# Optimization experiments

Hardware: AMD Instinct MI355X
Metric: run time of the kernel (lower is better)

The kernel has to match this reference:

```python
import jax, jax.numpy as jnp
import numpy as np

EMBED = 768
E2 = EMBED // 2  # 384
B = 128
T = 256   # 16x16 search tokens
T1 = 64   # 8x8 template tokens
EPS = 1e-5


def setup_inputs() -> dict:
    key = jax.random.key(0)
    ks = jax.random.split(key, 8)
    s = 0.02
    return {
        "z_r": jax.random.normal(ks[0], (B, T1, EMBED), jnp.float32),
        "z_i": jax.random.normal(ks[1], (B, T1, EMBED), jnp.float32),
        "x_r": jax.random.normal(ks[2], (B, T, EMBED), jnp.float32),
        "x_i": jax.random.normal(ks[3], (B, T, EMBED), jnp.float32),
        "fz_w": jax.random.normal(ks[4], (E2, 2 * EMBED), jnp.float32) * s,
        "fz_b": jnp.zeros((E2,), jnp.float32),
        "ln_g": jnp.ones((E2,), jnp.float32),
        "ln_b": jnp.zeros((E2,), jnp.float32),
        "wr": jax.random.normal(ks[5], (E2, EMBED, 3, 3), jnp.float32) * s,
        "br": jnp.zeros((E2,), jnp.float32),
        "bnr_g": jnp.ones((E2,), jnp.float32),
        "bnr_b": jnp.zeros((E2,), jnp.float32),
        "bnr_m": jnp.zeros((E2,), jnp.float32),
        "bnr_v": jnp.ones((E2,), jnp.float32),
        "wi": jax.random.normal(ks[6], (E2, EMBED, 3, 3), jnp.float32) * s,
        "bi": jnp.zeros((E2,), jnp.float32),
        "bni_g": jnp.ones((E2,), jnp.float32),
        "bni_b": jnp.zeros((E2,), jnp.float32),
        "bni_m": jnp.zeros((E2,), jnp.float32),
        "bni_v": jnp.ones((E2,), jnp.float32),
        "c": jnp.ones((1,), jnp.float32) * E2,
    }


def _gelu(x):
    return jax.nn.gelu(x, approximate=False)


def _layernorm(x, g, b):
    mu = jnp.mean(x, axis=-1, keepdims=True)
    var = jnp.mean(jnp.square(x - mu), axis=-1, keepdims=True)
    return (x - mu) * jax.lax.rsqrt(var + EPS) * g + b


def _conv_bn_gelu(x, w, b, g, beta, m, v):
    # x: [B, C_in, H, W], w: [C_out, C_in, 3, 3]; BN in eval mode (running stats)
    y = jax.lax.conv_general_dilated(
        x, w, window_strides=(1, 1), padding=((1, 1), (1, 1)),
        dimension_numbers=("NCHW", "OIHW", "NCHW"))
    y = y + b[None, :, None, None]
    y = (y - m[None, :, None, None]) * jax.lax.rsqrt(v[None, :, None, None] + EPS)
    y = y * g[None, :, None, None] + beta[None, :, None, None]
    return _gelu(y)


def _xcorr_fast(x, kernel):
    # x: [B, C, H, W]; kernel: [B, C, kh, kw] -> per-sample valid correlation
    def one(xb, kb):
        return jax.lax.conv_general_dilated(
            xb[None], kb[None], window_strides=(1, 1), padding="VALID",
            dimension_numbers=("NCHW", "OIHW", "NCHW"))[0]
    return jax.vmap(one)(x, kernel)  # [B, 1, oh, ow]


def reference(z_r, z_i, x_r, x_i, fz_w, fz_b, ln_g, ln_b,
              wr, br, bnr_g, bnr_b, bnr_m, bnr_v,
              wi, bi, bni_g, bni_b, bni_m, bni_v, c):
    Bn, t, embed = x_r.shape
    t1 = z_r.shape[1]
    sq, sq1 = int(np.sqrt(t)), int(np.sqrt(t1))
    # f_z: Linear + LayerNorm + GELU on concat(z_r, z_i)
    z = jnp.concatenate((z_r, z_i), axis=2)          # [B, t1, 2*embed]
    z = jnp.einsum("bte,oe->bto", z, fz_w) + fz_b    # [B, t1, E2]
    z = _gelu(_layernorm(z, ln_g, ln_b))
    z_f = z.transpose(0, 2, 1).reshape(Bn, -1, sq1, sq1)  # [B, E2, 8, 8]
    # down_r / down_i on search features
    xr = x_r.transpose(0, 2, 1).reshape(Bn, embed, sq, sq)
    xi = x_i.transpose(0, 2, 1).reshape(Bn, embed, sq, sq)
    xr = _conv_bn_gelu(xr, wr, br, bnr_g, bnr_b, bnr_m, bnr_v)
    xi = _conv_bn_gelu(xi, wi, bi, bni_g, bni_b, bni_m, bni_v)
    # center crop 16x16 -> 8x8
    xr = xr[:, :, 4:-4, 4:-4]
    xi = xi[:, :, 4:-4, 4:-4]
    s1 = jax.nn.sigmoid(_xcorr_fast(xr, z_f) / c)
    s2 = jax.nn.sigmoid(_xcorr_fast(xi, z_f) / c)
    return (s1, s2)
```

## Files before the change

kernel.cpp:

```cpp
#include <hip/hip_runtime.h>
#include <hip/hip_bf16.h>
#include <math.h>

#define EPSF 1e-5f

typedef __bf16 v8bf __attribute__((ext_vector_type(8)));
typedef float  v4f  __attribute__((ext_vector_type(4)));
typedef unsigned int u32;
typedef unsigned short u16;

__device__ __forceinline__ float gelu_exact(float x) {
    return 0.5f * x * (1.0f + erff(x * 0.70710678f));
}
__device__ __forceinline__ u16 f2bf(float f) {
    u32 u = __float_as_uint(f);
    return (u16)((u + 0x7fffu + ((u >> 16) & 1u)) >> 16);
}
__device__ __forceinline__ float bf2f(u16 u) {
    return __uint_as_float(((u32)u) << 16);
}
__device__ __forceinline__ void gload16(const void* g, void* l) {
    __builtin_amdgcn_global_load_lds((const __attribute__((address_space(1))) u32*)g,
                                     (__attribute__((address_space(3))) u32*)l, 16, 0, 0);
}

#define BARRIER(N) do { \
    asm volatile("s_waitcnt vmcnt(" #N ") lgkmcnt(0)" ::: "memory"); \
    __builtin_amdgcn_s_barrier(); \
} while (0)

__global__ __launch_bounds__(256) void kprep_z(const float* __restrict__ fz_w,
                                               u16* __restrict__ Bz) {
    int idx = blockIdx.x * 256 + threadIdx.x;
    int n = idx / 192;
    int r = idx % 192;
    int ec2 = r >> 2;
    int h = r & 3;
    const float* src = fz_w + (size_t)n * 1536 + ec2 * 32 + h * 8;
    float4 v0 = *(const float4*)src;
    float4 v1 = *(const float4*)(src + 4);
    uint4 pk;
    pk.x = (u32)f2bf(v0.x) | ((u32)f2bf(v0.y) << 16);
    pk.y = (u32)f2bf(v0.z) | ((u32)f2bf(v0.w) << 16);
    pk.z = (u32)f2bf(v1.x) | ((u32)f2bf(v1.y) << 16);
    pk.w = (u32)f2bf(v1.z) | ((u32)f2bf(v1.w) << 16);
    size_t slot = ((size_t)(ec2 * 4 + h) * 384 + n);
    *(uint4*)(Bz + slot * 8) = pk;
}

__global__ __launch_bounds__(256) void kprep_w(const float* __restrict__ wr,
                                               const float* __restrict__ wi,
                                               u16* __restrict__ Bw) {
    __shared__ float wsm[6912];
    const int tid = threadIdx.x;
    const int n = blockIdx.x >> 1;
    const int conv = blockIdx.x & 1;
    const float* w = (conv ? wi : wr) + (size_t)n * 6912;
#pragma unroll
    for (int k = 0; k < 7; ++k) {
        int sl = tid + k * 256;
        if (sl < 1728) ((float4*)wsm)[sl] = ((const float4*)w)[sl];
    }
    __syncthreads();
#pragma unroll
    for (int k = 0; k < 4; ++k) {
        int sl = tid + k * 256;
        if (sl < 864) {
            int h = sl & 3;
            int r = sl >> 2;
            int ec2 = r % 24;
            int s = r / 24;
            int ch0 = ec2 * 32 + h * 8;
            u16 tmp[8];
#pragma unroll
            for (int e = 0; e < 8; ++e) tmp[e] = f2bf(wsm[(ch0 + e) * 9 + s]);
            uint4 pk;
            pk.x = (u32)tmp[0] | ((u32)tmp[1] << 16);
            pk.y = (u32)tmp[2] | ((u32)tmp[3] << 16);
            pk.z = (u32)tmp[4] | ((u32)tmp[5] << 16);
            pk.w = (u32)tmp[6] | ((u32)tmp[7] << 16);
            size_t slot = ((size_t)conv * 864 + sl) * 384 + n;
            *(uint4*)(Bw + slot * 8) = pk;
        }
    }
}

#define ZB_BUF 24576
#define ZA_BUF 2048

__global__ __launch_bounds__(384, 1) void kz2(const float* __restrict__ z_r,
                                              const float* __restrict__ z_i,
                                              const u16* __restrict__ Bz,
                                              const float* __restrict__ fz_b,
                                              const float* __restrict__ ln_g,
                                              const float* __restrict__ ln_b,
                                              u16* __restrict__ zpk) {
    const int th = blockIdx.x;
    const int b  = blockIdx.y;
    const int tid  = threadIdx.x;
    const int lane = tid & 63;
    const int wid  = tid >> 6;
    const int l15  = lane & 15;
    const int h    = lane >> 4;

    __shared__ __align__(16) char lds[3 * ZB_BUF + 2 * ZA_BUF];
    char* ldsZB = lds;
    char* ldsZA = lds + 3 * ZB_BUF;
    __shared__ float redS[6 * 32], redQ[6 * 32], mu_s[32], rs_s[32];

    const float* zr_b = z_r + (size_t)b * (64 * 768);
    const float* zi_b = z_i + (size_t)b * (64 * 768);

    int boff[4];
#pragma unroll
    for (int nj = 0; nj < 4; ++nj) {
        int n = wid * 64 + nj * 16 + l15;
        boff[nj] = h * 6144 + n * 16;
    }
    int zaoff[2];
#pragma unroll
    for (int mi = 0; mi < 2; ++mi)
        zaoff[mi] = h * 512 + (mi * 16 + l15) * 16;

    auto stageZB = [&](int ec2, char* buf) {
        const char* src = (const char*)(Bz + (size_t)ec2 * 1536 * 8);
#pragma unroll
        for (int k = 0; k < 4; ++k) {
            int sl = tid + k * 384;
            gload16(src + sl * 16, buf + sl * 16);
        }
    };
    auto issueZA = [&](int ec2, float4* zr) {
        const float* zsrc = (ec2 < 24) ? zr_b : zi_b;
        const int ch0 = (ec2 < 24 ? ec2 : ec2 - 24) * 32;
        int sl = tid & 255;
        int row = sl >> 3, qq = sl & 7;
        zr[0] = *(const float4*)(zsrc + (size_t)(th * 32 + row) * 768 + ch0 + qq * 4);
    };
    auto convertZA = [&](const float4* zr, char* buf) {
        int sl = tid & 255;
        int row = sl >> 3, qq = sl & 7;
        ushort4 pk;
        pk.x = f2bf(zr[0].x); pk.y = f2bf(zr[0].y);
        pk.z = f2bf(zr[0].z); pk.w = f2bf(zr[0].w);
        *(ushort4*)(buf + (qq >> 1) * 512 + row * 16 + (qq & 1) * 8) = pk;
    };

    v4f acc[2][4] = {};

    auto comp = [&](char* curA, char* curB) {
        v8bf a[2], bfv[4];
#pragma unroll
        for (int mi = 0; mi < 2; ++mi) a[mi] = *(const v8bf*)(curA + zaoff[mi]);
#pragma unroll
        for (int nj = 0; nj < 4; ++nj) bfv[nj] = *(const v8bf*)(curB + boff[nj]);
        __builtin_amdgcn_s_setprio(1);
#pragma unroll
        for (int mi = 0; mi < 2; ++mi)
#pragma unroll
            for (int nj = 0; nj < 4; ++nj)
                acc[mi][nj] = __builtin_amdgcn_mfma_f32_16x16x32_bf16(a[mi], bfv[nj], acc[mi][nj], 0, 0, 0);
        __builtin_amdgcn_s_setprio(0);
    };

    float4 zreg[1];
    {
        issueZA(0, zreg);
        stageZB(0, ldsZB);
        stageZB(1, ldsZB + ZB_BUF);
        convertZA(zreg, ldsZA);
        issueZA(1, zreg);
        BARRIER(5);
    }
#pragma unroll 1
    for (int t = 0; t < 46; ++t) {
        stageZB(t + 2, ldsZB + ((t + 2) % 3) * ZB_BUF);
        comp(ldsZA + (t & 1) * ZA_BUF, ldsZB + (t % 3) * ZB_BUF);
        convertZA(zreg, ldsZA + ((t + 1) & 1) * ZA_BUF);
        issueZA(t + 2, zreg);
        BARRIER(5);
    }
    {
        comp(ldsZA + (46 & 1) * ZA_BUF, ldsZB + (46 % 3) * ZB_BUF);
        convertZA(zreg, ldsZA + (47 & 1) * ZA_BUF);
        BARRIER(0);
    }
    comp(ldsZA + (47 & 1) * ZA_BUF, ldsZB + (47 % 3) * ZB_BUF);

    float fzb[4], lng[4], lnb[4];
#pragma unroll
    for (int nj = 0; nj < 4; ++nj) {
        int o = wid * 64 + nj * 16 + l15;
        fzb[nj] = fz_b[o]; lng[nj] = ln_g[o]; lnb[nj] = ln_b[o];
    }
#pragma unroll
    for (int mi = 0; mi < 2; ++mi)
#pragma unroll
        for (int nj = 0; nj < 4; ++nj)
#pragma unroll
            for (int reg = 0; reg < 4; ++reg)
                acc[mi][nj][reg] += fzb[nj];

#pragma unroll
    for (int mi = 0; mi < 2; ++mi) {
#pragma unroll
        for (int reg = 0; reg < 4; ++reg) {
            float s = 0.f, q = 0.f;
#pragma unroll
            for (int nj = 0; nj < 4; ++nj) {
                float v = acc[mi][nj][reg];
                s += v; q += v * v;
            }
#pragma unroll
            for (int m = 0; m < 4; ++m) {
                s += __shfl_xor(s, 1 << m, 64);
                q += __shfl_xor(q, 1 << m, 64);
            }
            if (l15 == 0) {
                int row = mi * 16 + h * 4 + reg;
                redS[wid * 32 + row] = s;
                redQ[wid * 32 + row] = q;
            }
        }
    }
    __syncthreads();
    if (tid < 32) {
        float s = 0.f, q = 0.f;
#pragma unroll
        for (int w6 = 0; w6 < 6; ++w6) { s += redS[w6 * 32 + tid]; q += redQ[w6 * 32 + tid]; }
        float mu = s * (1.0f / 384.0f);
        float var = q * (1.0f / 384.0f) - mu * mu;
        mu_s[tid] = mu;
        rs_s[tid] = rsqrtf(var + EPSF);
    }
    __syncthreads();

#pragma unroll
    for (int mi = 0; mi < 2; ++mi)
#pragma unroll
        for (int nj = 0; nj < 4; ++nj) {
            int o = wid * 64 + nj * 16 + l15;
            u32* dst = (u32*)zpk + ((size_t)b * 384 + o) * 32 + th * 16 + mi * 8 + h * 2;
#pragma unroll
            for (int rp = 0; rp < 2; ++rp) {
                float zv[2];
#pragma unroll
                for (int k = 0; k < 2; ++k) {
                    int reg = rp * 2 + k;
                    int row = mi * 16 + h * 4 + reg;
                    float v = (acc[mi][nj][reg] - mu_s[row]) * rs_s[row] * lng[nj] + lnb[nj];
                    zv[k] = gelu_exact(v);
                }
                dst[rp] = (u32)f2bf(zv[0]) | ((u32)f2bf(zv[1]) << 16);
            }
        }
}

#define APL11  2848
#define ABUF11 (4 * APL11)
#define SSTRIDE 589824
#define ESTRIDE 24576

__global__ __launch_bounds__(384, 3) void kc11(const float* __restrict__ x_r,
                                               const float* __restrict__ x_i,
                                               const u16* __restrict__ Bw,
                                               const u16* __restrict__ zpk,
                                               const float* __restrict__ br,  const float* __restrict__ bnr_g,
                                               const float* __restrict__ bnr_b, const float* __restrict__ bnr_m,
                                               const float* __restrict__ bnr_v,
                                               const float* __restrict__ bi,  const float* __restrict__ bni_g,
                                               const float* __restrict__ bni_b, const float* __restrict__ bni_m,
                                               const float* __restrict__ bni_v,
                                               float* __restrict__ part) {
    const int q    = blockIdx.x;
    const int conv = q >> 1;
    const int nh   = q & 1;
    const int b    = blockIdx.y;
    const int tid  = threadIdx.x;
    const int lane = tid & 63;
    const int wid  = tid >> 6;
    const int l15  = lane & 15;
    const int h    = lane >> 4;

    __shared__ __align__(16) char ldsA[2 * ABUF11];
    __shared__ float redF[6];

    const float* x  = conv ? x_i : x_r;
    const float* xb = x + (size_t)b * (256 * 768);

    const char* bbase = (const char*)(Bw + (size_t)conv * (864 * 384 * 8))
                      + (size_t)h * 6144 + (nh * 192 + wid * 32 + l15) * 16;

    int aoff[4];
#pragma unroll
    for (int mi = 0; mi < 4; ++mi) {
        int p = mi * 16 + l15;
        int i = p >> 3, j = p & 7;
        aoff[mi] = h * APL11 + (i * 16 + j + 3) * 16;
    }

    auto issueA = [&](int ec2, float4* ar) {
#pragma unroll
        for (int k = 0; k < 4; ++k) {
            int sl = tid + k * 384;
            if (sl >= 1408) sl -= 1408;
            int row = sl >> 3, qq = sl & 7;
            ar[k] = *(const float4*)(xb + (size_t)(48 + row) * 768 + ec2 * 32 + qq * 4);
        }
    };
    auto convertA = [&](const float4* ar, char* buf) {
#pragma unroll
        for (int k = 0; k < 4; ++k) {
            int sl = tid + k * 384;
            if (sl >= 1408) sl -= 1408;
            int row = sl >> 3, qq = sl & 7;
            ushort4 pk;
            pk.x = f2bf(ar[k].x); pk.y = f2bf(ar[k].y);
            pk.z = f2bf(ar[k].z); pk.w = f2bf(ar[k].w);
            *(ushort4*)(buf + (qq >> 1) * APL11 + row * 16 + (qq & 1) * 8) = pk;
        }
    };

    v4f acc[4][2] = {};
    v8bf bpipe[6][2];
    float4 areg[4];

    {
        issueA(0, areg);
#pragma unroll
        for (int i = 0; i < 6; ++i) {
            const char* p = bbase + (size_t)i * SSTRIDE;
            bpipe[i][0] = *(const v8bf*)p;
            bpipe[i][1] = *(const v8bf*)(p + 256);
        }
        convertA(areg, ldsA);
        BARRIER(12);
    }

#define TAPC(S) do { \
        v8bf b0 = bpipe[(S) % 6][0]; \
        v8bf b1 = bpipe[(S) % 6][1]; \
        const int _so = (((S) / 3) * 16 + ((S) % 3)) * 16; \
        v8bf a0 = *(const v8bf*)(Acur + aoff[0] + _so); \
        v8bf a1 = *(const v8bf*)(Acur + aoff[1] + _so); \
        v8bf a2 = *(const v8bf*)(Acur + aoff[2] + _so); \
        v8bf a3 = *(const v8bf*)(Acur + aoff[3] + _so); \
        __builtin_amdgcn_s_setprio(1); \
        acc[0][0] = __builtin_amdgcn_mfma_f32_16x16x32_bf16(a0, b0, acc[0][0], 0, 0, 0); \
        acc[0][1] = __builtin_amdgcn_mfma_f32_16x16x32_bf16(a0, b1, acc[0][1], 0, 0, 0); \
        acc[1][0] = __builtin_amdgcn_mfma_f32_16x16x32_bf16(a1, b0, acc[1][0], 0, 0, 0); \
        acc[1][1] = __builtin_amdgcn_mfma_f32_16x16x32_bf16(a1, b1, acc[1][1], 0, 0, 0); \
        acc[2][0] = __builtin_amdgcn_mfma_f32_16x16x32_bf16(a2, b0, acc[2][0], 0, 0, 0); \
        acc[2][1] = __builtin_amdgcn_mfma_f32_16x16x32_bf16(a2, b1, acc[2][1], 0, 0, 0); \
        acc[3][0] = __builtin_amdgcn_mfma_f32_16x16x32_bf16(a3, b0, acc[3][0], 0, 0, 0); \
        acc[3][1] = __builtin_amdgcn_mfma_f32_16x16x32_bf16(a3, b1, acc[3][1], 0, 0, 0); \
        __builtin_amdgcn_s_setprio(0); \
        if ((S) <= 2) { \
            const char* _p = bptr + (size_t)((S) + 6) * SSTRIDE; \
            bpipe[(S) % 6][0] = *(const v8bf*)_p; \
            bpipe[(S) % 6][1] = *(const v8bf*)(_p + 256); \
        } else if (e < 23) { \
            const char* _p = bptr + ESTRIDE + (size_t)((S) - 3) * SSTRIDE; \
            bpipe[(S) % 6][0] = *(const v8bf*)_p; \
            bpipe[(S) % 6][1] = *(const v8bf*)(_p + 256); \
        } \
    } while (0)

#pragma unroll 1
    for (int e = 0; e < 24; ++e) {
        const char* Acur = ldsA + (e & 1) * ABUF11;
        const char* bptr = bbase + (size_t)e * ESTRIDE;
        TAPC(0); TAPC(1); TAPC(2);
        if (e < 23) issueA(e + 1, areg);
        TAPC(3); TAPC(4); TAPC(5); TAPC(6);
        if (e < 23) convertA(areg, ldsA + ((e + 1) & 1) * ABUF11);
        TAPC(7); TAPC(8);
        if (e < 23) BARRIER(12);
    }
#undef TAPC

    const float* bcp = conv ? bi    : br;
    const float* gp  = conv ? bni_g : bnr_g;
    const float* bbp = conv ? bni_b : bnr_b;
    const float* mp  = conv ? bni_m : bnr_m;
    const float* vp  = conv ? bni_v : bnr_v;

    float sum = 0.f;
#pragma unroll
    for (int nj = 0; nj < 2; ++nj) {
        const int o = nh * 192 + wid * 32 + nj * 16 + l15;
        const float sc  = gp[o] * rsqrtf(vp[o] + EPSF);
        const float sh2 = (bcp[o] - mp[o]) * sc + bbp[o];
        const u16* zb = zpk + ((size_t)b * 384 + o) * 64;
#pragma unroll
        for (int mi = 0; mi < 4; ++mi) {
            ushort4 zw = *(const ushort4*)(zb + mi * 16 + h * 4);
#pragma unroll
            for (int reg = 0; reg < 4; ++reg) {
                float y = fmaf(acc[mi][nj][reg], sc, sh2);
                u16 zu = (reg == 0) ? zw.x : (reg == 1) ? zw.y : (reg == 2) ? zw.z : zw.w;
                sum = fmaf(gelu_exact(y), bf2f(zu), sum);
            }
        }
    }
#pragma unroll
    for (int off = 32; off >= 1; off >>= 1) sum += __shfl_down(sum, off, 64);

    if (lane == 0) redF[wid] = sum;
    __syncthreads();
    if (tid == 0) {
        float t = redF[0] + redF[1] + redF[2] + redF[3] + redF[4] + redF[5];
        part[((size_t)conv * 128 + b) * 2 + nh] = t;
    }
}

__global__ __launch_bounds__(256) void kr(const float* __restrict__ part,
                                          const float* __restrict__ c,
                                          float* __restrict__ out) {
    int v = threadIdx.x;
    float s = part[v * 2] + part[v * 2 + 1];
    out[v] = 1.f / (1.f + expf(-s / c[0]));
}

extern "C" void kernel_launch(void* const* d_in, const int* in_sizes, int n_in,
                              void* d_out, int out_size, void* d_ws, size_t ws_size,
                              hipStream_t stream) {
    const float* z_r   = (const float*)d_in[0];
    const float* z_i   = (const float*)d_in[1];
    const float* x_r   = (const float*)d_in[2];
    const float* x_i   = (const float*)d_in[3];
    const float* fz_w  = (const float*)d_in[4];
    const float* fz_b  = (const float*)d_in[5];
    const float* ln_g  = (const float*)d_in[6];
    const float* ln_b  = (const float*)d_in[7];
    const float* wr    = (const float*)d_in[8];
    const float* br    = (const float*)d_in[9];
    const float* bnr_g = (const float*)d_in[10];
    const float* bnr_b = (const float*)d_in[11];
    const float* bnr_m = (const float*)d_in[12];
    const float* bnr_v = (const float*)d_in[13];
    const float* wi    = (const float*)d_in[14];
    const float* bi    = (const float*)d_in[15];
    const float* bni_g = (const float*)d_in[16];
    const float* bni_b = (const float*)d_in[17];
    const float* bni_m = (const float*)d_in[18];
    const float* bni_v = (const float*)d_in[19];
    const float* c     = (const float*)d_in[20];

    u16*   Bz   = (u16*)d_ws;
    u16*   Bw   = (u16*)((char*)d_ws + 1179648);
    u16*   zpk  = (u16*)((char*)d_ws + 1179648 + 10616832);
    float* part = (float*)((char*)d_ws + 1179648 + 10616832 + 6291456);

    kprep_z<<<288, 256, 0, stream>>>(fz_w, Bz);
    kprep_w<<<768, 256, 0, stream>>>(wr, wi, Bw);
    kz2<<<dim3(2, 128), 384, 0, stream>>>(z_r, z_i, Bz, fz_b, ln_g, ln_b, zpk);
    kc11<<<dim3(4, 128), 384, 0, stream>>>(x_r, x_i, Bw, zpk,
                                           br, bnr_g, bnr_b, bnr_m, bnr_v,
                                           bi, bni_g, bni_b, bni_m, bni_v,
                                           part);
    kr<<<1, 256, 0, stream>>>(part, c, (float*)d_out);
}
```

Before: 182.3 us.

## Merge output-channel halves into one 768-thread block per conv and batch

The conv kernel now launches one 768-thread block (12 waves) per (conv, batch) that covers all 384 output channels, where before two 384-thread blocks each covered half. The staged bf16 input tile in LDS is therefore loaded and converted once per sample instead of twice, halving that global traffic and conversion work. The B-operand register prefetch depth drops from 6 to 3 taps to fit more waves, and the partial-sum reduction is simplified. The risks are fewer blocks in flight (256 instead of 512), heavier barriers across 12 waves, and less latency hiding on weight loads.

```diff
diff --git a/kernel.cpp b/kernel.cpp
--- a/kernel.cpp
+++ b/kernel.cpp
@@ -256,12 +256,12 @@
         }
 }
 
-#define APL11  2848
-#define ABUF11 (4 * APL11)
-#define SSTRIDE 589824
-#define ESTRIDE 24576
-
-__global__ __launch_bounds__(384, 3) void kc11(const float* __restrict__ x_r,
+#define APL14  2816
+#define ABUF14 (4 * APL14)
+#define SSTR14 589824
+#define ESTR14 24576
+
+__global__ __launch_bounds__(768, 3) void kc14(const float* __restrict__ x_r,
                                                const float* __restrict__ x_i,
                                                const u16* __restrict__ Bw,
                                                const u16* __restrict__ zpk,
@@ -272,9 +272,7 @@
                                                const float* __restrict__ bni_b, const float* __restrict__ bni_m,
                                                const float* __restrict__ bni_v,
                                                float* __restrict__ part) {
-    const int q    = blockIdx.x;
-    const int conv = q >> 1;
-    const int nh   = q & 1;
+    const int conv = blockIdx.x;
     const int b    = blockIdx.y;
     const int tid  = threadIdx.x;
     const int lane = tid & 63;
@@ -282,27 +280,27 @@
     const int l15  = lane & 15;
     const int h    = lane >> 4;
 
-    __shared__ __align__(16) char ldsA[2 * ABUF11];
-    __shared__ float redF[6];
+    __shared__ __align__(16) char ldsA[2 * ABUF14];
+    __shared__ float redF[12];
 
     const float* x  = conv ? x_i : x_r;
     const float* xb = x + (size_t)b * (256 * 768);
 
     const char* bbase = (const char*)(Bw + (size_t)conv * (864 * 384 * 8))
-                      + (size_t)h * 6144 + (nh * 192 + wid * 32 + l15) * 16;
+                      + (size_t)h * 6144 + (wid * 32 + l15) * 16;
 
     int aoff[4];
 #pragma unroll
     for (int mi = 0; mi < 4; ++mi) {
         int p = mi * 16 + l15;
         int i = p >> 3, j = p & 7;
-        aoff[mi] = h * APL11 + (i * 16 + j + 3) * 16;
+        aoff[mi] = h * APL14 + (i * 16 + j + 3) * 16;
     }
 
     auto issueA = [&](int ec2, float4* ar) {
 #pragma unroll
-        for (int k = 0; k < 4; ++k) {
-            int sl = tid + k * 384;
+        for (int k = 0; k < 2; ++k) {
+            int sl = tid + k * 768;
             if (sl >= 1408) sl -= 1408;
             int row = sl >> 3, qq = sl & 7;
             ar[k] = *(const float4*)(xb + (size_t)(48 + row) * 768 + ec2 * 32 + qq * 4);
@@ -310,36 +308,36 @@
     };
     auto convertA = [&](const float4* ar, char* buf) {
 #pragma unroll
-        for (int k = 0; k < 4; ++k) {
-            int sl = tid + k * 384;
+        for (int k = 0; k < 2; ++k) {
+            int sl = tid + k * 768;
             if (sl >= 1408) sl -= 1408;
             int row = sl >> 3, qq = sl & 7;
             ushort4 pk;
             pk.x = f2bf(ar[k].x); pk.y = f2bf(ar[k].y);
             pk.z = f2bf(ar[k].z); pk.w = f2bf(ar[k].w);
-            *(ushort4*)(buf + (qq >> 1) * APL11 + row * 16 + (qq & 1) * 8) = pk;
+            *(ushort4*)(buf + (qq >> 1) * APL14 + row * 16 + (qq & 1) * 8) = pk;
         }
     };
 
     v4f acc[4][2] = {};
-    v8bf bpipe[6][2];
-    float4 areg[4];
+    v8bf bpipe[3][2];
+    float4 areg[2];
 
     {
         issueA(0, areg);
 #pragma unroll
-        for (int i = 0; i < 6; ++i) {
-            const char* p = bbase + (size_t)i * SSTRIDE;
+        for (int i = 0; i < 3; ++i) {
+            const char* p = bbase + (size_t)i * SSTR14;
             bpipe[i][0] = *(const v8bf*)p;
             bpipe[i][1] = *(const v8bf*)(p + 256);
         }
         convertA(areg, ldsA);
-        BARRIER(12);
-    }
-
-#define TAPC(S) do { \
-        v8bf b0 = bpipe[(S) % 6][0]; \
-        v8bf b1 = bpipe[(S) % 6][1]; \
+        BARRIER(6);
+    }
+
+#define TAP(S) do { \
+        v8bf b0 = bpipe[(S) % 3][0]; \
+        v8bf b1 = bpipe[(S) % 3][1]; \
         const int _so = (((S) / 3) * 16 + ((S) % 3)) * 16; \
         v8bf a0 = *(const v8bf*)(Acur + aoff[0] + _so); \
         v8bf a1 = *(const v8bf*)(Acur + aoff[1] + _so); \
@@ -355,29 +353,29 @@
         acc[3][0] = __builtin_amdgcn_mfma_f32_16x16x32_bf16(a3, b0, acc[3][0], 0, 0, 0); \
         acc[3][1] = __builtin_amdgcn_mfma_f32_16x16x32_bf16(a3, b1, acc[3][1], 0, 0, 0); \
         __builtin_amdgcn_s_setprio(0); \
-        if ((S) <= 2) { \
-            const char* _p = bptr + (size_t)((S) + 6) * SSTRIDE; \
-            bpipe[(S) % 6][0] = *(const v8bf*)_p; \
-            bpipe[(S) % 6][1] = *(const v8bf*)(_p + 256); \
+        if ((S) <= 5) { \
+            const char* _p = bptr + (size_t)((S) + 3) * SSTR14; \
+            bpipe[(S) % 3][0] = *(const v8bf*)_p; \
+            bpipe[(S) % 3][1] = *(const v8bf*)(_p + 256); \
         } else if (e < 23) { \
-            const char* _p = bptr + ESTRIDE + (size_t)((S) - 3) * SSTRIDE; \
-            bpipe[(S) % 6][0] = *(const v8bf*)_p; \
-            bpipe[(S) % 6][1] = *(const v8bf*)(_p + 256); \
+            const char* _p = bptr + ESTR14 + (size_t)((S) - 6) * SSTR14; \
+            bpipe[(S) % 3][0] = *(const v8bf*)_p; \
+            bpipe[(S) % 3][1] = *(const v8bf*)(_p + 256); \
         } \
     } while (0)
 
 #pragma unroll 1
     for (int e = 0; e < 24; ++e) {
-        const char* Acur = ldsA + (e & 1) * ABUF11;
-        const char* bptr = bbase + (size_t)e * ESTRIDE;
-        TAPC(0); TAPC(1); TAPC(2);
+        const char* Acur = ldsA + (e & 1) * ABUF14;
+        const char* bptr = bbase + (size_t)e * ESTR14;
+        TAP(0); TAP(1); TAP(2);
         if (e < 23) issueA(e + 1, areg);
-        TAPC(3); TAPC(4); TAPC(5); TAPC(6);
-        if (e < 23) convertA(areg, ldsA + ((e + 1) & 1) * ABUF11);
-        TAPC(7); TAPC(8);
-        if (e < 23) BARRIER(12);
-    }
-#undef TAPC
+        TAP(3); TAP(4); TAP(5); TAP(6);
+        if (e < 23) convertA(areg, ldsA + ((e + 1) & 1) * ABUF14);
+        TAP(7); TAP(8);
+        if (e < 23) BARRIER(6);
+    }
+#undef TAP
 
     const float* bcp = conv ? bi    : br;
     const float* gp  = conv ? bni_g : bnr_g;
@@ -388,7 +386,7 @@
     float sum = 0.f;
 #pragma unroll
     for (int nj = 0; nj < 2; ++nj) {
-        const int o = nh * 192 + wid * 32 + nj * 16 + l15;
+        const int o = wid * 32 + nj * 16 + l15;
         const float sc  = gp[o] * rsqrtf(vp[o] + EPSF);
         const float sh2 = (bcp[o] - mp[o]) * sc + bbp[o];
         const u16* zb = zpk + ((size_t)b * 384 + o) * 64;
@@ -409,8 +407,10 @@
     if (lane == 0) redF[wid] = sum;
     __syncthreads();
     if (tid == 0) {
-        float t = redF[0] + redF[1] + redF[2] + redF[3] + redF[4] + redF[5];
-        part[((size_t)conv * 128 + b) * 2 + nh] = t;
+        float t = 0.f;
+#pragma unroll
+        for (int w12 = 0; w12 < 12; ++w12) t += redF[w12];
+        part[(size_t)conv * 128 + b] = t;
     }
 }
 
@@ -418,8 +418,7 @@
                                           const float* __restrict__ c,
                                           float* __restrict__ out) {
     int v = threadIdx.x;
-    float s = part[v * 2] + part[v * 2 + 1];
-    out[v] = 1.f / (1.f + expf(-s / c[0]));
+    out[v] = 1.f / (1.f + expf(-part[v] / c[0]));
 }
 
 extern "C" void kernel_launch(void* const* d_in, const int* in_sizes, int n_in,
@@ -455,7 +454,7 @@
     kprep_z<<<288, 256, 0, stream>>>(fz_w, Bz);
     kprep_w<<<768, 256, 0, stream>>>(wr, wi, Bw);
     kz2<<<dim3(2, 128), 384, 0, stream>>>(z_r, z_i, Bz, fz_b, ln_g, ln_b, zpk);
-    kc11<<<dim3(4, 128), 384, 0, stream>>>(x_r, x_i, Bw, zpk,
+    kc14<<<dim3(2, 128), 768, 0, stream>>>(x_r, x_i, Bw, zpk,
                                            br, bnr_g, bnr_b, bnr_m, bnr_v,
                                            bi, bni_g, bni_b, bni_m, bni_v,
                                            part);
```

Result: faster. 163.9 us (median of 2 runs) (-10.1%).
